# Kernel tuning notes

Measured on AMD Instinct MI355X. Metric: run time of the kernel, lower is better.

Reference implementation:

```python
import jax, jax.numpy as jnp
import numpy as np

EPS = 1e-8
NUM_ITERATIONS = 3


def squash(t):
    # t: [..., out_channels]
    sq = jnp.sum(t * t, axis=-1, keepdims=True)
    return (sq / (1.0 + sq)) * t / jnp.sqrt(sq + EPS)


def setup_inputs() -> dict:
    key = jax.random.key(0)
    k1, k2 = jax.random.split(key)
    B, R, C, O, I = 512, 1152, 10, 16, 8
    x = jax.random.normal(k1, (B, R, I), dtype=jnp.float32)
    W = jax.random.normal(k2, (1, R, C, O, I), dtype=jnp.float32)
    return {"x": x, "W": W}


def reference(x, W):
    # x: [B, R, I]; W: [1, R, C, O, I]
    # u_hat[b,r,c,o] = sum_i W[0,r,c,o,i] * x[b,r,i]
    u_hat = jnp.einsum('rcoi,bri->brco', W[0], x)  # [B, R, C, O]
    B, R, C, _ = u_hat.shape
    b_ij = jnp.zeros((B, R, C, 1), dtype=u_hat.dtype)
    v_j = None
    for it in range(NUM_ITERATIONS):
        c_ij = jax.nn.softmax(b_ij, axis=2)              # softmax over capsules
        s_j = jnp.sum(c_ij * u_hat, axis=1, keepdims=True)  # [B, 1, C, O]
        v_j = squash(s_j)
        if it < NUM_ITERATIONS - 1:
            a_ij = jnp.sum(u_hat * v_j, axis=-1, keepdims=True)  # [B, R, C, 1]
            b_ij = b_ij + a_ij
    return jnp.squeeze(v_j, axis=1)  # [B, C, O]
```

## Files before the change

kernel.cpp:

```cpp
#include <hip/hip_runtime.h>

#define B_DIM 512
#define R_DIM 1152
#define C_DIM 10
#define CO    160
#define NCO4  40
#define NB    8
#define NCH   64
#define RPC   18

__device__ __forceinline__ float4 einsum8(const float* w, const float* xr)
{
    float4 acc = make_float4(0.f, 0.f, 0.f, 0.f);
    #pragma unroll
    for (int i = 0; i < 8; ++i) {
        acc.x = fmaf(w[i],      xr[i], acc.x);
        acc.y = fmaf(w[8 + i],  xr[i], acc.y);
        acc.z = fmaf(w[16 + i], xr[i], acc.z);
        acc.w = fmaf(w[24 + i], xr[i], acc.w);
    }
    return acc;
}

__global__ __launch_bounds__(256)
void k_sum(const float* __restrict__ x, const float* __restrict__ W,
           float* __restrict__ part)
{
    const int lane = threadIdx.x & 63;
    const int wv   = __builtin_amdgcn_readfirstlane((int)(threadIdx.x >> 6));
    const int co4  = (lane < NCO4) ? lane : lane - NCO4;
    const int b0   = (blockIdx.x * 4 + wv) * NB;
    const int r0   = blockIdx.y * RPC;

    const float* wp = W + (size_t)r0 * (CO * 8) + co4 * 32;
    float4 sacc[NB];
    #pragma unroll
    for (int i = 0; i < NB; ++i) sacc[i] = make_float4(0.f, 0.f, 0.f, 0.f);

    for (int rr = 0; rr < RPC; ++rr) {
        float w[32];
        #pragma unroll
        for (int k = 0; k < 8; ++k)
            *reinterpret_cast<float4*>(&w[k * 4]) =
                *reinterpret_cast<const float4*>(wp + k * 4);
        #pragma unroll
        for (int bb = 0; bb < NB; ++bb) {
            const float* xq = x + ((size_t)(b0 + bb) * R_DIM + r0 + rr) * 8;
            float xr[8];
            *reinterpret_cast<float4*>(&xr[0]) = *reinterpret_cast<const float4*>(xq);
            *reinterpret_cast<float4*>(&xr[4]) = *reinterpret_cast<const float4*>(xq + 4);
            float4 u4 = einsum8(w, xr);
            sacc[bb].x += u4.x; sacc[bb].y += u4.y;
            sacc[bb].z += u4.z; sacc[bb].w += u4.w;
        }
        wp += CO * 8;
    }
    if (lane < NCO4) {
        #pragma unroll
        for (int bb = 0; bb < NB; ++bb)
            *reinterpret_cast<float4*>(
                part + ((size_t)blockIdx.y * B_DIM + b0 + bb) * CO + co4 * 4) = sacc[bb];
    }
}

template<int PASS>
__global__ __launch_bounds__(256)
void k_pass(const float* __restrict__ x, const float* __restrict__ W,
            const float* __restrict__ v1, const float* __restrict__ v2,
            float* __restrict__ part)
{
    const int lane = threadIdx.x & 63;
    const int wv   = __builtin_amdgcn_readfirstlane((int)(threadIdx.x >> 6));
    const int co4  = (lane < NCO4) ? lane : lane - NCO4;
    const int b0   = (blockIdx.x * 4 + wv) * NB;
    const int r0   = blockIdx.y * RPC;

    float4 vl[NB];
    #pragma unroll
    for (int bb = 0; bb < NB; ++bb) {
        float4 a = *reinterpret_cast<const float4*>(
            v1 + (size_t)(b0 + bb) * CO + co4 * 4);
        if constexpr (PASS == 2) {
            float4 b2 = *reinterpret_cast<const float4*>(
                v2 + (size_t)(b0 + bb) * CO + co4 * 4);
            a.x += b2.x; a.y += b2.y; a.z += b2.z; a.w += b2.w;
        }
        vl[bb] = a;
    }

    float4 sacc[NB];
    #pragma unroll
    for (int i = 0; i < NB; ++i) sacc[i] = make_float4(0.f, 0.f, 0.f, 0.f);

    const float* wp = W + (size_t)r0 * (CO * 8) + co4 * 32;
    for (int rr = 0; rr < RPC; ++rr) {
        float w[32];
        #pragma unroll
        for (int k = 0; k < 8; ++k)
            *reinterpret_cast<float4*>(&w[k * 4]) =
                *reinterpret_cast<const float4*>(wp + k * 4);
        #pragma unroll
        for (int bb = 0; bb < NB; ++bb) {
            const float* xq = x + ((size_t)(b0 + bb) * R_DIM + r0 + rr) * 8;
            float xr[8];
            *reinterpret_cast<float4*>(&xr[0]) = *reinterpret_cast<const float4*>(xq);
            *reinterpret_cast<float4*>(&xr[4]) = *reinterpret_cast<const float4*>(xq + 4);
            float4 u4 = einsum8(w, xr);

            float p = u4.x * vl[bb].x + u4.y * vl[bb].y
                    + u4.z * vl[bb].z + u4.w * vl[bb].w;
            p += __shfl_xor(p, 1);
            p += __shfl_xor(p, 2);

            float m = p;
            m = fmaxf(m, __shfl_xor(m, 4));
            m = fmaxf(m, __shfl_xor(m, 8));
            m = fmaxf(m, __shfl_xor(m, 16));
            m = fmaxf(m, __shfl_xor(m, 32));

            float e = (lane < NCO4) ? __expf(p - m) : 0.f;
            float Z = e;
            Z += __shfl_xor(Z, 4);
            Z += __shfl_xor(Z, 8);
            Z += __shfl_xor(Z, 16);
            Z += __shfl_xor(Z, 32);

            const float cij = e / Z;
            sacc[bb].x += cij * u4.x; sacc[bb].y += cij * u4.y;
            sacc[bb].z += cij * u4.z; sacc[bb].w += cij * u4.w;
        }
        wp += CO * 8;
    }

    if (lane < NCO4) {
        #pragma unroll
        for (int bb = 0; bb < NB; ++bb)
            *reinterpret_cast<float4*>(
                part + ((size_t)blockIdx.y * B_DIM + b0 + bb) * CO + co4 * 4) = sacc[bb];
    }
}

__global__ __launch_bounds__(256)
void k_vred(const float* __restrict__ part, float* __restrict__ dst,
            int nchunk, float scale)
{
    const int idx = blockIdx.x * 256 + threadIdx.x;
    const int b = idx / CO, co = idx % CO;
    float s = 0.f;
    for (int k = 0; k < nchunk; ++k)
        s += part[((size_t)k * B_DIM + b) * CO + co];
    s *= scale;
    float sq = s * s;
    sq += __shfl_xor(sq, 1);
    sq += __shfl_xor(sq, 2);
    sq += __shfl_xor(sq, 4);
    sq += __shfl_xor(sq, 8);
    float v = s * (sq / (1.f + sq)) / sqrtf(sq + 1e-8f);
    dst[idx] = v;
}

extern "C" void kernel_launch(void* const* d_in, const int* in_sizes, int n_in,
                              void* d_out, int out_size, void* d_ws, size_t ws_size,
                              hipStream_t stream)
{
    const float* x = (const float*)d_in[0];
    const float* W = (const float*)d_in[1];
    float* out = (float*)d_out;
    float* ws  = (float*)d_ws;

    const size_t NP = (size_t)NCH * B_DIM * CO;
    const size_t NV = (size_t)B_DIM * CO;
    if (ws_size < (3 * NP + 2 * NV) * 4) return;

    float* part1 = ws;
    float* part2 = part1 + NP;
    float* part3 = part2 + NP;
    float* v1    = part3 + NP;
    float* v2    = v1    + NV;

    const dim3 G(16, NCH), T(256), GV(320), TV(256);
    k_sum    <<<G, T, 0, stream>>>(x, W, part1);
    k_vred   <<<GV, TV, 0, stream>>>(part1, v1, NCH, 0.1f);
    k_pass<1><<<G, T, 0, stream>>>(x, W, v1, v1, part2);
    k_vred   <<<GV, TV, 0, stream>>>(part2, v2, NCH, 1.0f);
    k_pass<2><<<G, T, 0, stream>>>(x, W, v1, v2, part3);
    k_vred   <<<GV, TV, 0, stream>>>(part3, out, NCH, 1.0f);
}
```

Measured before the change: 409.9 us.

## Drop softmax max, use ds_swizzle reductions, halve per-wave batch in routing passes

Removes the max-subtraction reduction from the capsule softmax, since routing logits stay bounded, and replaces most cross-lane shuffles with cheaper ds_swizzle ops. The routing-pass kernels now handle 4 batches per wave on a grid twice as large, with occupancy launch bounds to cut register pressure. X pointers are advanced incrementally, and a fast divide is used for the softmax normalisation. Dropping the max relies on logits never overflowing exp.

```diff
diff --git a/kernel.cpp b/kernel.cpp
--- a/kernel.cpp
+++ b/kernel.cpp
@@ -5,9 +5,10 @@
 #define C_DIM 10
 #define CO    160
 #define NCO4  40
-#define NB    8
 #define NCH   64
 #define RPC   18
+
+#define SWZ(v, mask) __int_as_float(__builtin_amdgcn_ds_swizzle(__float_as_int(v), 0x1F | ((mask) << 10)))
 
 __device__ __forceinline__ float4 einsum8(const float* w, const float* xr)
 {
@@ -22,20 +23,25 @@
     return acc;
 }
 
-__global__ __launch_bounds__(256)
+__global__ __launch_bounds__(256, 4)
 void k_sum(const float* __restrict__ x, const float* __restrict__ W,
            float* __restrict__ part)
 {
     const int lane = threadIdx.x & 63;
-    const int wv   = __builtin_amdgcn_readfirstlane((int)(threadIdx.x >> 6));
+    const int wv   = threadIdx.x >> 6;
     const int co4  = (lane < NCO4) ? lane : lane - NCO4;
-    const int b0   = (blockIdx.x * 4 + wv) * NB;
+    const int b0   = (blockIdx.x * 4 + wv) * 8;
     const int r0   = blockIdx.y * RPC;
 
     const float* wp = W + (size_t)r0 * (CO * 8) + co4 * 32;
-    float4 sacc[NB];
+    const float* xp[8];
     #pragma unroll
-    for (int i = 0; i < NB; ++i) sacc[i] = make_float4(0.f, 0.f, 0.f, 0.f);
+    for (int bb = 0; bb < 8; ++bb)
+        xp[bb] = x + ((size_t)(b0 + bb) * R_DIM + r0) * 8;
+
+    float4 sacc[8];
+    #pragma unroll
+    for (int i = 0; i < 8; ++i) sacc[i] = make_float4(0.f, 0.f, 0.f, 0.f);
 
     for (int rr = 0; rr < RPC; ++rr) {
         float w[32];
@@ -44,11 +50,11 @@
             *reinterpret_cast<float4*>(&w[k * 4]) =
                 *reinterpret_cast<const float4*>(wp + k * 4);
         #pragma unroll
-        for (int bb = 0; bb < NB; ++bb) {
-            const float* xq = x + ((size_t)(b0 + bb) * R_DIM + r0 + rr) * 8;
+        for (int bb = 0; bb < 8; ++bb) {
             float xr[8];
-            *reinterpret_cast<float4*>(&xr[0]) = *reinterpret_cast<const float4*>(xq);
-            *reinterpret_cast<float4*>(&xr[4]) = *reinterpret_cast<const float4*>(xq + 4);
+            *reinterpret_cast<float4*>(&xr[0]) = *reinterpret_cast<const float4*>(xp[bb]);
+            *reinterpret_cast<float4*>(&xr[4]) = *reinterpret_cast<const float4*>(xp[bb] + 4);
+            xp[bb] += 8;
             float4 u4 = einsum8(w, xr);
             sacc[bb].x += u4.x; sacc[bb].y += u4.y;
             sacc[bb].z += u4.z; sacc[bb].w += u4.w;
@@ -57,27 +63,27 @@
     }
     if (lane < NCO4) {
         #pragma unroll
-        for (int bb = 0; bb < NB; ++bb)
+        for (int bb = 0; bb < 8; ++bb)
             *reinterpret_cast<float4*>(
                 part + ((size_t)blockIdx.y * B_DIM + b0 + bb) * CO + co4 * 4) = sacc[bb];
     }
 }
 
 template<int PASS>
-__global__ __launch_bounds__(256)
+__global__ __launch_bounds__(256, 4)
 void k_pass(const float* __restrict__ x, const float* __restrict__ W,
             const float* __restrict__ v1, const float* __restrict__ v2,
             float* __restrict__ part)
 {
     const int lane = threadIdx.x & 63;
-    const int wv   = __builtin_amdgcn_readfirstlane((int)(threadIdx.x >> 6));
+    const int wv   = threadIdx.x >> 6;
     const int co4  = (lane < NCO4) ? lane : lane - NCO4;
-    const int b0   = (blockIdx.x * 4 + wv) * NB;
+    const int b0   = (blockIdx.x * 4 + wv) * 4;
     const int r0   = blockIdx.y * RPC;
 
-    float4 vl[NB];
+    float4 vl[4];
     #pragma unroll
-    for (int bb = 0; bb < NB; ++bb) {
+    for (int bb = 0; bb < 4; ++bb) {
         float4 a = *reinterpret_cast<const float4*>(
             v1 + (size_t)(b0 + bb) * CO + co4 * 4);
         if constexpr (PASS == 2) {
@@ -88,11 +94,16 @@
         vl[bb] = a;
     }
 
-    float4 sacc[NB];
+    const float* wp = W + (size_t)r0 * (CO * 8) + co4 * 32;
+    const float* xp[4];
     #pragma unroll
-    for (int i = 0; i < NB; ++i) sacc[i] = make_float4(0.f, 0.f, 0.f, 0.f);
+    for (int bb = 0; bb < 4; ++bb)
+        xp[bb] = x + ((size_t)(b0 + bb) * R_DIM + r0) * 8;
 
-    const float* wp = W + (size_t)r0 * (CO * 8) + co4 * 32;
+    float4 sacc[4];
+    #pragma unroll
+    for (int i = 0; i < 4; ++i) sacc[i] = make_float4(0.f, 0.f, 0.f, 0.f);
+
     for (int rr = 0; rr < RPC; ++rr) {
         float w[32];
         #pragma unroll
@@ -100,32 +111,26 @@
             *reinterpret_cast<float4*>(&w[k * 4]) =
                 *reinterpret_cast<const float4*>(wp + k * 4);
         #pragma unroll
-        for (int bb = 0; bb < NB; ++bb) {
-            const float* xq = x + ((size_t)(b0 + bb) * R_DIM + r0 + rr) * 8;
+        for (int bb = 0; bb < 4; ++bb) {
             float xr[8];
-            *reinterpret_cast<float4*>(&xr[0]) = *reinterpret_cast<const float4*>(xq);
-            *reinterpret_cast<float4*>(&xr[4]) = *reinterpret_cast<const float4*>(xq + 4);
+            *reinterpret_cast<float4*>(&xr[0]) = *reinterpret_cast<const float4*>(xp[bb]);
+            *reinterpret_cast<float4*>(&xr[4]) = *reinterpret_cast<const float4*>(xp[bb] + 4);
+            xp[bb] += 8;
             float4 u4 = einsum8(w, xr);
 
             float p = u4.x * vl[bb].x + u4.y * vl[bb].y
                     + u4.z * vl[bb].z + u4.w * vl[bb].w;
-            p += __shfl_xor(p, 1);
-            p += __shfl_xor(p, 2);
+            p += SWZ(p, 1);
+            p += SWZ(p, 2);
 
-            float m = p;
-            m = fmaxf(m, __shfl_xor(m, 4));
-            m = fmaxf(m, __shfl_xor(m, 8));
-            m = fmaxf(m, __shfl_xor(m, 16));
-            m = fmaxf(m, __shfl_xor(m, 32));
-
-            float e = (lane < NCO4) ? __expf(p - m) : 0.f;
+            float e = (lane < NCO4) ? __expf(p) : 0.f;
             float Z = e;
-            Z += __shfl_xor(Z, 4);
-            Z += __shfl_xor(Z, 8);
-            Z += __shfl_xor(Z, 16);
+            Z += SWZ(Z, 4);
+            Z += SWZ(Z, 8);
+            Z += SWZ(Z, 16);
             Z += __shfl_xor(Z, 32);
 
-            const float cij = e / Z;
+            const float cij = __fdividef(e, Z);
             sacc[bb].x += cij * u4.x; sacc[bb].y += cij * u4.y;
             sacc[bb].z += cij * u4.z; sacc[bb].w += cij * u4.w;
         }
@@ -134,7 +139,7 @@
 
     if (lane < NCO4) {
         #pragma unroll
-        for (int bb = 0; bb < NB; ++bb)
+        for (int bb = 0; bb < 4; ++bb)
             *reinterpret_cast<float4*>(
                 part + ((size_t)blockIdx.y * B_DIM + b0 + bb) * CO + co4 * 4) = sacc[bb];
     }
@@ -151,10 +156,10 @@
         s += part[((size_t)k * B_DIM + b) * CO + co];
     s *= scale;
     float sq = s * s;
-    sq += __shfl_xor(sq, 1);
-    sq += __shfl_xor(sq, 2);
-    sq += __shfl_xor(sq, 4);
-    sq += __shfl_xor(sq, 8);
+    sq += SWZ(sq, 1);
+    sq += SWZ(sq, 2);
+    sq += SWZ(sq, 4);
+    sq += SWZ(sq, 8);
     float v = s * (sq / (1.f + sq)) / sqrtf(sq + 1e-8f);
     dst[idx] = v;
 }
@@ -178,11 +183,11 @@
     float* v1    = part3 + NP;
     float* v2    = v1    + NV;
 
-    const dim3 G(16, NCH), T(256), GV(320), TV(256);
-    k_sum    <<<G, T, 0, stream>>>(x, W, part1);
-    k_vred   <<<GV, TV, 0, stream>>>(part1, v1, NCH, 0.1f);
-    k_pass<1><<<G, T, 0, stream>>>(x, W, v1, v1, part2);
-    k_vred   <<<GV, TV, 0, stream>>>(part2, v2, NCH, 1.0f);
-    k_pass<2><<<G, T, 0, stream>>>(x, W, v1, v2, part3);
-    k_vred   <<<GV, TV, 0, stream>>>(part3, out, NCH, 1.0f);
+    const dim3 GS(16, NCH), GP(32, NCH), T(256), GV(320);
+    k_sum    <<<GS, T, 0, stream>>>(x, W, part1);
+    k_vred   <<<GV, T, 0, stream>>>(part1, v1, NCH, 0.1f);
+    k_pass<1><<<GP, T, 0, stream>>>(x, W, v1, v1, part2);
+    k_vred   <<<GV, T, 0, stream>>>(part2, v2, NCH, 1.0f);
+    k_pass<2><<<GP, T, 0, stream>>>(x, W, v1, v2, part3);
+    k_vred   <<<GV, T, 0, stream>>>(part3, out, NCH, 1.0f);
 }
```

Result: slower. 539.9 us (+31.7%).
